# Kernel optimization log

Hardware: AMD Instinct MI355X
Metric: run time of the kernel (lower is better)

The kernel has to match this reference:

```python
import jax, jax.numpy as jnp
import numpy as np

NUM_EXPERTS = 8
TOP_K = 2
HIDDEN = 2048
INTER = 1024
B, S = 4, 1024


def setup_inputs() -> dict:
    key = jax.random.key(0)
    ks = jax.random.split(key, 5)
    sx = 1.0 / np.sqrt(HIDDEN)
    si = 1.0 / np.sqrt(INTER)
    return {
        "x": jax.random.normal(ks[0], (B, S, HIDDEN), dtype=jnp.float32),
        # router gate: Linear(hidden -> num_experts), weight stored [E, H] (torch convention)
        "gate_w": jax.random.normal(ks[1], (NUM_EXPERTS, HIDDEN), dtype=jnp.float32) * sx,
        # stacked expert weights: gate/up [E, I, H], down [E, H, I]
        "gate_proj_w": jax.random.normal(ks[2], (NUM_EXPERTS, INTER, HIDDEN), dtype=jnp.float32) * sx,
        "up_proj_w": jax.random.normal(ks[3], (NUM_EXPERTS, INTER, HIDDEN), dtype=jnp.float32) * sx,
        "down_proj_w": jax.random.normal(ks[4], (NUM_EXPERTS, HIDDEN, INTER), dtype=jnp.float32) * si,
    }


def _moe_forward(x, gate_w, gate_proj_w, up_proj_w, down_proj_w):
    Bx, Sx, H = x.shape
    T = Bx * Sx
    h = x.reshape(T, H)
    # --- routing (Qwen3: softmax in fp32, top-k, renormalize) ---
    router_logits = h @ gate_w.T                                   # [T, E]
    probs = jax.nn.softmax(router_logits.astype(jnp.float32), axis=-1)
    top_vals, top_idx = jax.lax.top_k(probs, TOP_K)                # [T, K]
    top_vals = top_vals / jnp.sum(top_vals, axis=-1, keepdims=True)  # norm_topk_prob
    # dense routing weights [T, E]: zero for unselected experts
    rw = jnp.zeros((T, NUM_EXPERTS), dtype=jnp.float32)
    rw = rw.at[jnp.arange(T)[:, None], top_idx].add(top_vals)
    rw = rw.astype(h.dtype)
    # --- SwiGLU experts, computed densely and masked by routing weights ---
    g = jnp.einsum('th,eih->tei', h, gate_proj_w)                  # [T, E, I]
    u = jnp.einsum('th,eih->tei', h, up_proj_w)                    # [T, E, I]
    a = jax.nn.silu(g) * u                                         # [T, E, I]
    out_e = jnp.einsum('tei,ehi->teh', a, down_proj_w)             # [T, E, H]
    out = jnp.einsum('te,teh->th', rw, out_e)                      # [T, H]
    return out.reshape(Bx, Sx, H)


def reference(x, gate_w, gate_proj_w, up_proj_w, down_proj_w):
    return _moe_forward(x, gate_w, gate_proj_w, up_proj_w, down_proj_w)
```

## Files before the change

### kernel.cpp

```cpp
#include <hip/hip_runtime.h>
#include <hip/hip_bf16.h>

#define NUM_EXPERTS 8
#define HIDDEN 2048
#define INTER 1024
#define T_TOKENS 4096
#define NSLOTS (T_TOKENS * 2)

#define BM 128
#define BN 128
#define BK 32

typedef __attribute__((ext_vector_type(8))) short short8;
typedef __attribute__((ext_vector_type(4))) float f32x4;

__device__ __forceinline__ ushort f2bf(float f) {
    __hip_bfloat16 h = __float2bfloat16(f);
    return *reinterpret_cast<ushort*>(&h);
}

__device__ __forceinline__ void load_lds16(const void* g, void* lds) {
    __builtin_amdgcn_global_load_lds(
        (const __attribute__((address_space(1))) void*)g,
        (__attribute__((address_space(3))) void*)lds, 16, 0, 0);
}

__global__ __launch_bounds__(256) void cvt_bf16(const float* __restrict__ in,
                                                ushort* __restrict__ out, int n4) {
    int i = blockIdx.x * 256 + threadIdx.x;
    int stride = gridDim.x * 256;
    for (; i < n4; i += stride) {
        float4 v = reinterpret_cast<const float4*>(in)[i];
        ushort4 o;
        o.x = f2bf(v.x); o.y = f2bf(v.y); o.z = f2bf(v.z); o.w = f2bf(v.w);
        reinterpret_cast<ushort4*>(out)[i] = o;
    }
}

__global__ __launch_bounds__(64) void moe_router(const float* __restrict__ x,
                                                 const float* __restrict__ gw,
                                                 int* __restrict__ top_idx,
                                                 float* __restrict__ top_w,
                                                 int* __restrict__ counts) {
    int t = blockIdx.x;
    int lane = threadIdx.x;
    const float* xt = x + (size_t)t * HIDDEN;
    float acc[NUM_EXPERTS];
#pragma unroll
    for (int e = 0; e < NUM_EXPERTS; e++) acc[e] = 0.f;
    for (int h = lane; h < HIDDEN; h += 64) {
        float xv = xt[h];
#pragma unroll
        for (int e = 0; e < NUM_EXPERTS; e++)
            acc[e] = fmaf(xv, gw[e * HIDDEN + h], acc[e]);
    }
#pragma unroll
    for (int e = 0; e < NUM_EXPERTS; e++) {
#pragma unroll
        for (int off = 32; off > 0; off >>= 1)
            acc[e] += __shfl_xor(acc[e], off);
    }
    if (lane == 0) {
        int i1 = 0; float l1 = acc[0];
#pragma unroll
        for (int e = 1; e < NUM_EXPERTS; e++)
            if (acc[e] > l1) { l1 = acc[e]; i1 = e; }
        int i2 = -1; float l2 = -3.4e38f;
#pragma unroll
        for (int e = 0; e < NUM_EXPERTS; e++)
            if (e != i1 && acc[e] > l2) { l2 = acc[e]; i2 = e; }
        float w2 = __expf(l2 - l1);
        float denom = 1.f + w2;
        top_idx[t * 2 + 0] = i1;
        top_idx[t * 2 + 1] = i2;
        top_w[t * 2 + 0] = 1.f / denom;
        top_w[t * 2 + 1] = w2 / denom;
        atomicAdd(&counts[i1], 1);
        atomicAdd(&counts[i2], 1);
    }
}

__global__ void moe_offsets(const int* __restrict__ counts,
                            int* __restrict__ ebase, int* __restrict__ cursor) {
    if (threadIdx.x == 0 && blockIdx.x == 0) {
        int s = 0;
        for (int e = 0; e < NUM_EXPERTS; e++) {
            ebase[e] = s; cursor[e] = s; s += counts[e];
        }
    }
}

__global__ __launch_bounds__(256) void moe_scatter(const int* __restrict__ top_idx,
                                                   const float* __restrict__ top_w,
                                                   int* __restrict__ cursor,
                                                   int* __restrict__ slot_tok,
                                                   float* __restrict__ slot_w) {
    int t = blockIdx.x * 256 + threadIdx.x;
    if (t >= T_TOKENS) return;
#pragma unroll
    for (int k = 0; k < 2; k++) {
        int e = top_idx[t * 2 + k];
        int pos = atomicAdd(&cursor[e], 1);
        slot_tok[pos] = t;
        slot_w[pos] = top_w[t * 2 + k];
    }
}

__global__ __launch_bounds__(256) void moe_gateup(const ushort* __restrict__ xb,
                                                  const ushort* __restrict__ wgb,
                                                  const ushort* __restrict__ wub,
                                                  const int* __restrict__ slot_tok,
                                                  const int* __restrict__ ebase,
                                                  const int* __restrict__ ecnt,
                                                  ushort* __restrict__ act) {
    __shared__ ushort ldsA[BM * BK];
    __shared__ ushort ldsG[BN * BK];
    __shared__ ushort ldsU[BN * BK];

    const int e = blockIdx.z;
    const int bm = blockIdx.y;
    const int bn = blockIdx.x;
    const int cnt = ecnt[e];
    if (bm * BM >= cnt) return;
    const int b0 = ebase[e];

    const int tid = threadIdx.x;
    const int lane = tid & 63;
    const int wid = tid >> 6;
    const int wr = wid >> 1, wc = wid & 1;

    const int ar0 = bm * BM + (tid >> 2);
    const int ar1 = ar0 + 64;
    const int cl0 = (ar0 < cnt) ? ar0 : (cnt - 1);
    const int cl1 = (ar1 < cnt) ? ar1 : (cnt - 1);
    const int tok0 = slot_tok[b0 + cl0];
    const int tok1 = slot_tok[b0 + cl1];
    const int kc = (tid & 3) * 8;
    const ushort* pA0 = xb + (size_t)tok0 * HIDDEN + kc;
    const ushort* pA1 = xb + (size_t)tok1 * HIDDEN + kc;
    const size_t wrow0 = (size_t)e * INTER + (size_t)(bn * BN + (tid >> 2));
    const ushort* pG0 = wgb + wrow0 * HIDDEN + kc;
    const ushort* pG1 = pG0 + (size_t)64 * HIDDEN;
    const ushort* pU0 = wub + wrow0 * HIDDEN + kc;
    const ushort* pU1 = pU0 + (size_t)64 * HIDDEN;

    ushort* dA = ldsA + tid * 8;
    ushort* dG = ldsG + tid * 8;
    ushort* dU = ldsU + tid * 8;

    f32x4 accg[4][4] = {};
    f32x4 accu[4][4] = {};

    const int fr = lane & 15;
    const int fk = (lane >> 4) * 8;

    for (int kk = 0; kk < HIDDEN; kk += BK) {
        load_lds16(pA0, dA);
        load_lds16(pA1, dA + 2048);
        load_lds16(pG0, dG);
        load_lds16(pG1, dG + 2048);
        load_lds16(pU0, dU);
        load_lds16(pU1, dU + 2048);
        pA0 += BK; pA1 += BK; pG0 += BK; pG1 += BK; pU0 += BK; pU1 += BK;
        __syncthreads();

        short8 a[4], bg[4], bu[4];
#pragma unroll
        for (int m = 0; m < 4; m++)
            a[m] = *(const short8*)(ldsA + (wr * 64 + m * 16 + fr) * BK + fk);
#pragma unroll
        for (int n = 0; n < 4; n++) {
            bg[n] = *(const short8*)(ldsG + (wc * 64 + n * 16 + fr) * BK + fk);
            bu[n] = *(const short8*)(ldsU + (wc * 64 + n * 16 + fr) * BK + fk);
        }
#pragma unroll
        for (int m = 0; m < 4; m++) {
#pragma unroll
            for (int n = 0; n < 4; n++) {
                accg[m][n] = __builtin_amdgcn_mfma_f32_16x16x32_bf16(a[m], bg[n], accg[m][n], 0, 0, 0);
                accu[m][n] = __builtin_amdgcn_mfma_f32_16x16x32_bf16(a[m], bu[n], accu[m][n], 0, 0, 0);
            }
        }
        __syncthreads();
    }

#pragma unroll
    for (int m = 0; m < 4; m++) {
#pragma unroll
        for (int r = 0; r < 4; r++) {
            int row = bm * BM + wr * 64 + m * 16 + (lane >> 4) * 4 + r;
            if (row < cnt) {
                size_t arow = (size_t)(b0 + row) * INTER;
#pragma unroll
                for (int n = 0; n < 4; n++) {
                    int col = bn * BN + wc * 64 + n * 16 + (lane & 15);
                    float g = accg[m][n][r];
                    float u = accu[m][n][r];
                    float s = g / (1.f + __expf(-g));
                    act[arow + col] = f2bf(s * u);
                }
            }
        }
    }
}

__global__ __launch_bounds__(256) void moe_down(const ushort* __restrict__ act,
                                                const ushort* __restrict__ wdb,
                                                const int* __restrict__ slot_tok,
                                                const float* __restrict__ slot_w,
                                                const int* __restrict__ ebase,
                                                const int* __restrict__ ecnt,
                                                float* __restrict__ out) {
    __shared__ ushort ldsA[BM * BK];
    __shared__ ushort ldsB[BN * BK];

    const int e = blockIdx.z;
    const int bm = blockIdx.y;
    const int bn = blockIdx.x;
    const int cnt = ecnt[e];
    if (bm * BM >= cnt) return;
    const int b0 = ebase[e];

    const int tid = threadIdx.x;
    const int lane = tid & 63;
    const int wid = tid >> 6;
    const int wr = wid >> 1, wc = wid & 1;

    const int ar0 = bm * BM + (tid >> 2);
    const int ar1 = ar0 + 64;
    const int sr0 = b0 + ((ar0 < cnt) ? ar0 : (cnt - 1));
    const int sr1 = b0 + ((ar1 < cnt) ? ar1 : (cnt - 1));
    const int kc = (tid & 3) * 8;
    const ushort* pA0 = act + (size_t)sr0 * INTER + kc;
    const ushort* pA1 = act + (size_t)sr1 * INTER + kc;
    const size_t wrow = (size_t)e * HIDDEN + (size_t)(bn * BN + (tid >> 2));
    const ushort* pB0 = wdb + wrow * INTER + kc;
    const ushort* pB1 = pB0 + (size_t)64 * INTER;

    ushort* dA = ldsA + tid * 8;
    ushort* dB = ldsB + tid * 8;

    f32x4 acc[4][4] = {};

    const int fr = lane & 15;
    const int fk = (lane >> 4) * 8;

    for (int kk = 0; kk < INTER; kk += BK) {
        load_lds16(pA0, dA);
        load_lds16(pA1, dA + 2048);
        load_lds16(pB0, dB);
        load_lds16(pB1, dB + 2048);
        pA0 += BK; pA1 += BK; pB0 += BK; pB1 += BK;
        __syncthreads();

        short8 a[4], b[4];
#pragma unroll
        for (int m = 0; m < 4; m++)
            a[m] = *(const short8*)(ldsA + (wr * 64 + m * 16 + fr) * BK + fk);
#pragma unroll
        for (int n = 0; n < 4; n++)
            b[n] = *(const short8*)(ldsB + (wc * 64 + n * 16 + fr) * BK + fk);
#pragma unroll
        for (int m = 0; m < 4; m++) {
#pragma unroll
            for (int n = 0; n < 4; n++) {
                acc[m][n] = __builtin_amdgcn_mfma_f32_16x16x32_bf16(a[m], b[n], acc[m][n], 0, 0, 0);
            }
        }
        __syncthreads();
    }

#pragma unroll
    for (int m = 0; m < 4; m++) {
#pragma unroll
        for (int r = 0; r < 4; r++) {
            int row = bm * BM + wr * 64 + m * 16 + (lane >> 4) * 4 + r;
            if (row < cnt) {
                int slot = b0 + row;
                int tok = slot_tok[slot];
                float w = slot_w[slot];
                float* orow = out + (size_t)tok * HIDDEN;
#pragma unroll
                for (int n = 0; n < 4; n++) {
                    int col = bn * BN + wc * 64 + n * 16 + (lane & 15);
                    atomicAdd(&orow[col], acc[m][n][r] * w);
                }
            }
        }
    }
}

extern "C" void kernel_launch(void* const* d_in, const int* in_sizes, int n_in,
                              void* d_out, int out_size, void* d_ws, size_t ws_size,
                              hipStream_t stream) {
    const float* x  = (const float*)d_in[0];
    const float* gw = (const float*)d_in[1];
    const float* wg = (const float*)d_in[2];
    const float* wu = (const float*)d_in[3];
    const float* wd = (const float*)d_in[4];
    float* out = (float*)d_out;

    char* ws = (char*)d_ws;
    ushort* xb  = (ushort*)(ws);
    ushort* wgb = (ushort*)(ws + 16777216);
    ushort* wub = (ushort*)(ws + 16777216 + 33554432);
    ushort* wdb = (ushort*)(ws + 16777216 + 2u * 33554432);
    ushort* act = (ushort*)(ws + 16777216 + 3u * 33554432);
    char* p = ws + 2u * 16777216 + 3u * 33554432;
    int*   top_idx  = (int*)p;   p += 32768;
    float* top_w    = (float*)p; p += 32768;
    int*   slot_tok = (int*)p;   p += 32768;
    float* slot_w   = (float*)p; p += 32768;
    int*   counts   = (int*)p;   p += 128;
    int*   ebase    = (int*)p;   p += 128;
    int*   cursor   = (int*)p;   p += 128;

    hipMemsetAsync(counts, 0, 128, stream);
    hipMemsetAsync(d_out, 0, (size_t)out_size * sizeof(float), stream);

    cvt_bf16<<<1024, 256, 0, stream>>>(x,  xb,  (T_TOKENS * HIDDEN) / 4);
    cvt_bf16<<<1024, 256, 0, stream>>>(wg, wgb, (NUM_EXPERTS * INTER * HIDDEN) / 4);
    cvt_bf16<<<1024, 256, 0, stream>>>(wu, wub, (NUM_EXPERTS * INTER * HIDDEN) / 4);
    cvt_bf16<<<1024, 256, 0, stream>>>(wd, wdb, (NUM_EXPERTS * HIDDEN * INTER) / 4);

    moe_router<<<T_TOKENS, 64, 0, stream>>>(x, gw, top_idx, top_w, counts);
    moe_offsets<<<1, 64, 0, stream>>>(counts, ebase, cursor);
    moe_scatter<<<(T_TOKENS + 255) / 256, 256, 0, stream>>>(top_idx, top_w, cursor, slot_tok, slot_w);

    moe_gateup<<<dim3(INTER / BN, T_TOKENS / BM, NUM_EXPERTS), 256, 0, stream>>>(
        xb, wgb, wub, slot_tok, ebase, counts, act);
    moe_down<<<dim3(HIDDEN / BN, T_TOKENS / BM, NUM_EXPERTS), 256, 0, stream>>>(
        act, wdb, slot_tok, slot_w, ebase, counts, out);
}
```

Measured before the change: 695.1 us.

## Double-buffer LDS, swizzle layout, and shrink M tile in MoE GEMMs

Both expert GEMM kernels now double-buffer the LDS tiles so the next K-slice's global-to-LDS loads are issued before the current slice's MFMAs, with a single barrier per iteration. An XOR swizzle on the 16-byte column chunks is applied to cut LDS bank conflicts. The M tile shrinks from 128 to 64 and launch bounds request higher occupancy, aiming for more blocks and better latency hiding. The cost is less reuse of weight tiles per block, so weight traffic from L2 roughly doubles.

```diff
diff --git a/kernel.cpp b/kernel.cpp
--- a/kernel.cpp
+++ b/kernel.cpp
@@ -5,11 +5,12 @@
 #define HIDDEN 2048
 #define INTER 1024
 #define T_TOKENS 4096
-#define NSLOTS (T_TOKENS * 2)
-
-#define BM 128
-#define BN 128
+
 #define BK 32
+#define GU_BM 64
+#define GU_BN 128
+#define DN_BM 64
+#define DN_BN 128
 
 typedef __attribute__((ext_vector_type(8))) short short8;
 typedef __attribute__((ext_vector_type(4))) float f32x4;
@@ -106,22 +107,22 @@
     }
 }
 
-__global__ __launch_bounds__(256) void moe_gateup(const ushort* __restrict__ xb,
-                                                  const ushort* __restrict__ wgb,
-                                                  const ushort* __restrict__ wub,
-                                                  const int* __restrict__ slot_tok,
-                                                  const int* __restrict__ ebase,
-                                                  const int* __restrict__ ecnt,
-                                                  ushort* __restrict__ act) {
-    __shared__ ushort ldsA[BM * BK];
-    __shared__ ushort ldsG[BN * BK];
-    __shared__ ushort ldsU[BN * BK];
+__global__ __launch_bounds__(256, 3) void moe_gateup(const ushort* __restrict__ xb,
+                                                     const ushort* __restrict__ wgb,
+                                                     const ushort* __restrict__ wub,
+                                                     const int* __restrict__ slot_tok,
+                                                     const int* __restrict__ ebase,
+                                                     const int* __restrict__ ecnt,
+                                                     ushort* __restrict__ act) {
+    __shared__ ushort ldsA[2][GU_BM * BK];
+    __shared__ ushort ldsG[2][GU_BN * BK];
+    __shared__ ushort ldsU[2][GU_BN * BK];
 
     const int e = blockIdx.z;
     const int bm = blockIdx.y;
     const int bn = blockIdx.x;
     const int cnt = ecnt[e];
-    if (bm * BM >= cnt) return;
+    if (bm * GU_BM >= cnt) return;
     const int b0 = ebase[e];
 
     const int tid = threadIdx.x;
@@ -129,52 +130,55 @@
     const int wid = tid >> 6;
     const int wr = wid >> 1, wc = wid & 1;
 
-    const int ar0 = bm * BM + (tid >> 2);
-    const int ar1 = ar0 + 64;
-    const int cl0 = (ar0 < cnt) ? ar0 : (cnt - 1);
-    const int cl1 = (ar1 < cnt) ? ar1 : (cnt - 1);
-    const int tok0 = slot_tok[b0 + cl0];
-    const int tok1 = slot_tok[b0 + cl1];
-    const int kc = (tid & 3) * 8;
-    const ushort* pA0 = xb + (size_t)tok0 * HIDDEN + kc;
-    const ushort* pA1 = xb + (size_t)tok1 * HIDDEN + kc;
-    const size_t wrow0 = (size_t)e * INTER + (size_t)(bn * BN + (tid >> 2));
-    const ushort* pG0 = wgb + wrow0 * HIDDEN + kc;
+    const int r = tid >> 2, cs = tid & 3;
+    const int scl = (cs ^ ((r >> 1) & 3)) * 8;
+    const int ar = bm * GU_BM + r;
+    const int tok = slot_tok[b0 + ((ar < cnt) ? ar : (cnt - 1))];
+    const ushort* pA = xb + (size_t)tok * HIDDEN + scl;
+    const size_t wrow0 = (size_t)e * INTER + (size_t)(bn * GU_BN + r);
+    const ushort* pG0 = wgb + wrow0 * HIDDEN + scl;
     const ushort* pG1 = pG0 + (size_t)64 * HIDDEN;
-    const ushort* pU0 = wub + wrow0 * HIDDEN + kc;
+    const ushort* pU0 = wub + wrow0 * HIDDEN + scl;
     const ushort* pU1 = pU0 + (size_t)64 * HIDDEN;
 
-    ushort* dA = ldsA + tid * 8;
-    ushort* dG = ldsG + tid * 8;
-    ushort* dU = ldsU + tid * 8;
-
-    f32x4 accg[4][4] = {};
-    f32x4 accu[4][4] = {};
-
     const int fr = lane & 15;
-    const int fk = (lane >> 4) * 8;
-
-    for (int kk = 0; kk < HIDDEN; kk += BK) {
-        load_lds16(pA0, dA);
-        load_lds16(pA1, dA + 2048);
-        load_lds16(pG0, dG);
-        load_lds16(pG1, dG + 2048);
-        load_lds16(pU0, dU);
-        load_lds16(pU1, dU + 2048);
-        pA0 += BK; pA1 += BK; pG0 += BK; pG1 += BK; pU0 += BK; pU1 += BK;
-        __syncthreads();
-
-        short8 a[4], bg[4], bu[4];
-#pragma unroll
-        for (int m = 0; m < 4; m++)
-            a[m] = *(const short8*)(ldsA + (wr * 64 + m * 16 + fr) * BK + fk);
+    const int colsw = (((lane >> 4) ^ ((fr >> 1) & 3)) * 8);
+
+    f32x4 accg[2][4] = {};
+    f32x4 accu[2][4] = {};
+
+#define GU_STAGE(buf, t)                                              \
+    do {                                                              \
+        const int _o = (t) * BK;                                      \
+        load_lds16(pA + _o,  &ldsA[buf][tid * 8]);                    \
+        load_lds16(pG0 + _o, &ldsG[buf][tid * 8]);                    \
+        load_lds16(pG1 + _o, &ldsG[buf][2048 + tid * 8]);             \
+        load_lds16(pU0 + _o, &ldsU[buf][tid * 8]);                    \
+        load_lds16(pU1 + _o, &ldsU[buf][2048 + tid * 8]);             \
+    } while (0)
+
+    GU_STAGE(0, 0);
+    __syncthreads();
+
+    int cur = 0;
+    const int NT = HIDDEN / BK;
+    for (int t = 0; t < NT; ++t) {
+        if (t + 1 < NT) GU_STAGE(cur ^ 1, t + 1);
+
+        const ushort* LA = ldsA[cur];
+        const ushort* LG = ldsG[cur];
+        const ushort* LU = ldsU[cur];
+        short8 a[2], bg[4], bu[4];
+#pragma unroll
+        for (int m = 0; m < 2; m++)
+            a[m] = *(const short8*)(LA + (wr * 32 + m * 16 + fr) * BK + colsw);
 #pragma unroll
         for (int n = 0; n < 4; n++) {
-            bg[n] = *(const short8*)(ldsG + (wc * 64 + n * 16 + fr) * BK + fk);
-            bu[n] = *(const short8*)(ldsU + (wc * 64 + n * 16 + fr) * BK + fk);
-        }
-#pragma unroll
-        for (int m = 0; m < 4; m++) {
+            bg[n] = *(const short8*)(LG + (wc * 64 + n * 16 + fr) * BK + colsw);
+            bu[n] = *(const short8*)(LU + (wc * 64 + n * 16 + fr) * BK + colsw);
+        }
+#pragma unroll
+        for (int m = 0; m < 2; m++) {
 #pragma unroll
             for (int n = 0; n < 4; n++) {
                 accg[m][n] = __builtin_amdgcn_mfma_f32_16x16x32_bf16(a[m], bg[n], accg[m][n], 0, 0, 0);
@@ -182,20 +186,22 @@
             }
         }
         __syncthreads();
-    }
-
-#pragma unroll
-    for (int m = 0; m < 4; m++) {
-#pragma unroll
-        for (int r = 0; r < 4; r++) {
-            int row = bm * BM + wr * 64 + m * 16 + (lane >> 4) * 4 + r;
+        cur ^= 1;
+    }
+#undef GU_STAGE
+
+#pragma unroll
+    for (int m = 0; m < 2; m++) {
+#pragma unroll
+        for (int rr = 0; rr < 4; rr++) {
+            int row = bm * GU_BM + wr * 32 + m * 16 + (lane >> 4) * 4 + rr;
             if (row < cnt) {
                 size_t arow = (size_t)(b0 + row) * INTER;
 #pragma unroll
                 for (int n = 0; n < 4; n++) {
-                    int col = bn * BN + wc * 64 + n * 16 + (lane & 15);
-                    float g = accg[m][n][r];
-                    float u = accu[m][n][r];
+                    int col = bn * GU_BN + wc * 64 + n * 16 + fr;
+                    float g = accg[m][n][rr];
+                    float u = accu[m][n][rr];
                     float s = g / (1.f + __expf(-g));
                     act[arow + col] = f2bf(s * u);
                 }
@@ -204,21 +210,21 @@
     }
 }
 
-__global__ __launch_bounds__(256) void moe_down(const ushort* __restrict__ act,
-                                                const ushort* __restrict__ wdb,
-                                                const int* __restrict__ slot_tok,
-                                                const float* __restrict__ slot_w,
-                                                const int* __restrict__ ebase,
-                                                const int* __restrict__ ecnt,
-                                                float* __restrict__ out) {
-    __shared__ ushort ldsA[BM * BK];
-    __shared__ ushort ldsB[BN * BK];
+__global__ __launch_bounds__(256, 4) void moe_down(const ushort* __restrict__ act,
+                                                   const ushort* __restrict__ wdb,
+                                                   const int* __restrict__ slot_tok,
+                                                   const float* __restrict__ slot_w,
+                                                   const int* __restrict__ ebase,
+                                                   const int* __restrict__ ecnt,
+                                                   float* __restrict__ out) {
+    __shared__ ushort ldsA[2][DN_BM * BK];
+    __shared__ ushort ldsB[2][DN_BN * BK];
 
     const int e = blockIdx.z;
     const int bm = blockIdx.y;
     const int bn = blockIdx.x;
     const int cnt = ecnt[e];
-    if (bm * BM >= cnt) return;
+    if (bm * DN_BM >= cnt) return;
     const int b0 = ebase[e];
 
     const int tid = threadIdx.x;
@@ -226,55 +232,61 @@
     const int wid = tid >> 6;
     const int wr = wid >> 1, wc = wid & 1;
 
-    const int ar0 = bm * BM + (tid >> 2);
-    const int ar1 = ar0 + 64;
-    const int sr0 = b0 + ((ar0 < cnt) ? ar0 : (cnt - 1));
-    const int sr1 = b0 + ((ar1 < cnt) ? ar1 : (cnt - 1));
-    const int kc = (tid & 3) * 8;
-    const ushort* pA0 = act + (size_t)sr0 * INTER + kc;
-    const ushort* pA1 = act + (size_t)sr1 * INTER + kc;
-    const size_t wrow = (size_t)e * HIDDEN + (size_t)(bn * BN + (tid >> 2));
-    const ushort* pB0 = wdb + wrow * INTER + kc;
+    const int r = tid >> 2, cs = tid & 3;
+    const int scl = (cs ^ ((r >> 1) & 3)) * 8;
+    const int ar = bm * DN_BM + r;
+    const int sr = b0 + ((ar < cnt) ? ar : (cnt - 1));
+    const ushort* pA = act + (size_t)sr * INTER + scl;
+    const size_t wrow = (size_t)e * HIDDEN + (size_t)(bn * DN_BN + r);
+    const ushort* pB0 = wdb + wrow * INTER + scl;
     const ushort* pB1 = pB0 + (size_t)64 * INTER;
 
-    ushort* dA = ldsA + tid * 8;
-    ushort* dB = ldsB + tid * 8;
-
-    f32x4 acc[4][4] = {};
-
     const int fr = lane & 15;
-    const int fk = (lane >> 4) * 8;
-
-    for (int kk = 0; kk < INTER; kk += BK) {
-        load_lds16(pA0, dA);
-        load_lds16(pA1, dA + 2048);
-        load_lds16(pB0, dB);
-        load_lds16(pB1, dB + 2048);
-        pA0 += BK; pA1 += BK; pB0 += BK; pB1 += BK;
+    const int colsw = (((lane >> 4) ^ ((fr >> 1) & 3)) * 8);
+
+    f32x4 acc[2][4] = {};
+
+#define DN_STAGE(buf, t)                                              \
+    do {                                                              \
+        const int _o = (t) * BK;                                      \
+        load_lds16(pA + _o,  &ldsA[buf][tid * 8]);                    \
+        load_lds16(pB0 + _o, &ldsB[buf][tid * 8]);                    \
+        load_lds16(pB1 + _o, &ldsB[buf][2048 + tid * 8]);             \
+    } while (0)
+
+    DN_STAGE(0, 0);
+    __syncthreads();
+
+    int cur = 0;
+    const int NT = INTER / BK;
+    for (int t = 0; t < NT; ++t) {
+        if (t + 1 < NT) DN_STAGE(cur ^ 1, t + 1);
+
+        const ushort* LA = ldsA[cur];
+        const ushort* LB = ldsB[cur];
+        short8 a[2], b[4];
+#pragma unroll
+        for (int m = 0; m < 2; m++)
+            a[m] = *(const short8*)(LA + (wr * 32 + m * 16 + fr) * BK + colsw);
+#pragma unroll
+        for (int n = 0; n < 4; n++)
+            b[n] = *(const short8*)(LB + (wc * 64 + n * 16 + fr) * BK + colsw);
+#pragma unroll
+        for (int m = 0; m < 2; m++) {
+#pragma unroll
+            for (int n = 0; n < 4; n++)
+                acc[m][n] = __builtin_amdgcn_mfma_f32_16x16x32_bf16(a[m], b[n], acc[m][n], 0, 0, 0);
+        }
         __syncthreads();
-
-        short8 a[4], b[4];
-#pragma unroll
-        for (int m = 0; m < 4; m++)
-            a[m] = *(const short8*)(ldsA + (wr * 64 + m * 16 + fr) * BK + fk);
-#pragma unroll
-        for (int n = 0; n < 4; n++)
-            b[n] = *(const short8*)(ldsB + (wc * 64 + n * 16 + fr) * BK + fk);
-#pragma unroll
-        for (int m = 0; m < 4; m++) {
-#pragma unroll
-            for (int n = 0; n < 4; n++) {
-                acc[m][n] = __builtin_amdgcn_mfma_f32_16x16x32_bf16(a[m], b[n], acc[m][n], 0, 0, 0);
-            }
-        }
-        __syncthreads();
-    }
-
-#pragma unroll
-    for (int m = 0; m < 4; m++) {
-#pragma unroll
-        for (int r = 0; r < 4; r++) {
-            int row = bm * BM + wr * 64 + m * 16 + (lane >> 4) * 4 + r;
+        cur ^= 1;
+    }
+#undef DN_STAGE
+
+#pragma unroll
+    for (int m = 0; m < 2; m++) {
+#pragma unroll
+        for (int rr = 0; rr < 4; rr++) {
+            int row = bm * DN_BM + wr * 32 + m * 16 + (lane >> 4) * 4 + rr;
             if (row < cnt) {
                 int slot = b0 + row;
                 int tok = slot_tok[slot];
@@ -282,8 +294,8 @@
                 float* orow = out + (size_t)tok * HIDDEN;
 #pragma unroll
                 for (int n = 0; n < 4; n++) {
-                    int col = bn * BN + wc * 64 + n * 16 + (lane & 15);
-                    atomicAdd(&orow[col], acc[m][n][r] * w);
+                    int col = bn * DN_BN + wc * 64 + n * 16 + fr;
+                    atomicAdd(&orow[col], acc[m][n][rr] * w);
                 }
             }
         }
@@ -327,8 +339,8 @@
     moe_offsets<<<1, 64, 0, stream>>>(counts, ebase, cursor);
     moe_scatter<<<(T_TOKENS + 255) / 256, 256, 0, stream>>>(top_idx, top_w, cursor, slot_tok, slot_w);
 
-    moe_gateup<<<dim3(INTER / BN, T_TOKENS / BM, NUM_EXPERTS), 256, 0, stream>>>(
+    moe_gateup<<<dim3(INTER / GU_BN, T_TOKENS / GU_BM, NUM_EXPERTS), 256, 0, stream>>>(
         xb, wgb, wub, slot_tok, ebase, counts, act);
-    moe_down<<<dim3(HIDDEN / BN, T_TOKENS / BM, NUM_EXPERTS), 256, 0, stream>>>(
+    moe_down<<<dim3(HIDDEN / DN_BN, T_TOKENS / DN_BM, NUM_EXPERTS), 256, 0, stream>>>(
         act, wdb, slot_tok, slot_w, ebase, counts, out);
 }
```

After: 616.9 us. 11.2% less time.
